# Kernel optimization log

Hardware: AMD Instinct MI355X
Metric: run time of the kernel (lower is better)

Reference implementation:

```python
import jax, jax.numpy as jnp
import numpy as np

T_STEPS = 200
B = 512
D = 32
LMBD = 1.0


def _socm_const_m_loss(ts, states, noises, controls, nabla_V, nabla_f,
                       nabla_b, nabla_g, sigma, log_pd, log_ps, log_tw):
    # ts: [T+1]; states/nabla_V: [T+1,B,D]; noises/controls/nabla_f: [T,B,D];
    # nabla_b: [T,B,D,D]; nabla_g: [B,D]; sigma: [D,D]; logs: [B]
    sigma_inv_T = jnp.linalg.inv(sigma).T

    # integrand terms on the first T timesteps ([:-1] slice in torch source)
    term1 = nabla_f  # nabla_f(ts[0], states)[:-1]
    sig_noises = jnp.einsum('ij,abj->abi', sigma_inv_T, noises)
    term2 = -np.sqrt(LMBD) * jnp.einsum('abij,abj->abi', nabla_b, sig_noises)
    sig_controls = jnp.einsum('ij,abj->abi', sigma_inv_T, controls)
    term3 = -jnp.einsum('abij,abj->abi', nabla_b, sig_controls)

    dts = ts[1:] - ts[:-1]                      # [T]
    dts_ = dts[:, None, None]
    zeros = jnp.zeros_like(term1[:1])           # [1,B,D]

    t1_dt = jnp.concatenate([zeros, term1 * dts_], axis=0)             # [T+1,B,D]
    t2_sdt = jnp.concatenate([zeros, term2 * jnp.sqrt(dts_)], axis=0)
    t3_dt = jnp.concatenate([zeros, term3 * dts_], axis=0)

    def rev_cum(x):
        # total_sum - cumsum == reverse cumulative sum starting at each step
        return jnp.sum(x, axis=0, keepdims=True) - jnp.cumsum(x, axis=0)

    least_squares_target = (rev_cum(t1_dt) + rev_cum(t2_sdt) + rev_cum(t3_dt)
                            + nabla_g[None, :, :])                     # [T+1,B,D]

    control_learned = -jnp.einsum('ij,tbj->tbi', sigma.T, nabla_V)
    control_target = -jnp.einsum('ij,tbj->tbi', sigma.T, least_squares_target)

    weight = jnp.exp(log_pd + log_ps + log_tw)  # [B]
    sq = (control_learned - control_target) ** 2 * weight[None, :, None]
    n_t, n_b = states.shape[0], states.shape[1]
    return jnp.sum(sq) / (n_t * n_b)


def setup_inputs() -> dict:
    key = jax.random.key(0)
    ks = jax.random.split(key, 11)
    ts = jnp.linspace(0.0, 1.0, T_STEPS + 1, dtype=jnp.float32)
    states = jax.random.normal(ks[0], (T_STEPS + 1, B, D), jnp.float32)
    noises = jax.random.normal(ks[1], (T_STEPS, B, D), jnp.float32)
    controls = jax.random.normal(ks[2], (T_STEPS, B, D), jnp.float32)
    nabla_V = jax.random.normal(ks[3], (T_STEPS + 1, B, D), jnp.float32)
    nabla_f = jax.random.normal(ks[4], (T_STEPS, B, D), jnp.float32)
    nabla_b = 0.1 * jax.random.normal(ks[5], (T_STEPS, B, D, D), jnp.float32)
    nabla_g = jax.random.normal(ks[6], (B, D), jnp.float32)
    sigma = jnp.eye(D, dtype=jnp.float32) + 0.05 * jax.random.normal(ks[7], (D, D), jnp.float32)
    log_pd = 0.01 * jax.random.normal(ks[8], (B,), jnp.float32)
    log_ps = 0.01 * jax.random.normal(ks[9], (B,), jnp.float32)
    log_tw = 0.01 * jax.random.normal(ks[10], (B,), jnp.float32)
    return {"ts": ts, "states": states, "noises": noises, "controls": controls,
            "nabla_V": nabla_V, "nabla_f": nabla_f, "nabla_b": nabla_b,
            "nabla_g": nabla_g, "sigma": sigma, "log_pd": log_pd,
            "log_ps": log_ps, "log_tw": log_tw}


def reference(ts, states, noises, controls, nabla_V, nabla_f, nabla_b,
              nabla_g, sigma, log_pd, log_ps, log_tw):
    return _socm_const_m_loss(ts, states, noises, controls, nabla_V, nabla_f,
                              nabla_b, nabla_g, sigma, log_pd, log_ps, log_tw)
```

## Files before the change

kernel.cpp:

```cpp
#include <hip/hip_runtime.h>
#include <math.h>

#define T_STEPS 200
#define BB 512
#define DD 32
#define LMBD 1.0f
#define NCH 8
#define CHT 25

#define WS_MINV 0
#define WS_A    1024
#define WS_W    2048
#define WS_PART 2560
#define WS_DT   3072
#define WS_SDT  3328
#define WS_CT   4096
#define WS_Y    135168
#define WS_M    266240

__global__ __launch_bounds__(512) void prep_kernel(
    const float* __restrict__ ts,
    const float* __restrict__ sigma,
    const float* __restrict__ lpd, const float* __restrict__ lps,
    const float* __restrict__ ltw,
    float* __restrict__ ws)
{
    __shared__ float sg[32][33];
    const int tid = threadIdx.x;

    ws[WS_W + tid] = expf(lpd[tid] + lps[tid] + ltw[tid]);

    if (tid < T_STEPS) {
        float a = ts[tid], b = ts[tid + 1];
        float dt = b - a;
        ws[WS_DT + tid]  = dt;
        ws[WS_SDT + tid] = sqrtf(LMBD * dt);
    }

    for (int idx = tid; idx < 1024; idx += 512)
        sg[idx >> 5][idx & 31] = sigma[idx];
    __syncthreads();

    for (int idx = tid; idx < 1024; idx += 512) {
        int i = idx >> 5, j = idx & 31;
        float s = 0.0f;
        #pragma unroll
        for (int k = 0; k < 32; ++k) s += sg[i][k] * sg[j][k];
        ws[WS_A + idx] = s;
    }

    if (tid < 64) {
        const int l = tid;
        float col[32];
        #pragma unroll
        for (int r = 0; r < 32; ++r) {
            float v = sg[r][l & 31];
            col[r] = (l < 32) ? v : ((r == (l - 32)) ? 1.0f : 0.0f);
        }
        #pragma unroll
        for (int k = 0; k < 32; ++k) {
            float pinv = 1.0f / __shfl(col[k], k);
            col[k] *= pinv;
            #pragma unroll
            for (int r = 0; r < 32; ++r) {
                if (r == k) continue;
                float f = __shfl(col[r], k);
                col[r] -= f * col[k];
            }
        }
        if (l >= 32) {
            #pragma unroll
            for (int r = 0; r < 32; ++r)
                ws[WS_MINV + (l - 32) * 32 + r] = col[r];
        }
    }
}

__global__ __launch_bounds__(64) void stream_kernel(
    const float* __restrict__ noises,
    const float* __restrict__ controls,
    const float* __restrict__ nabla_f,
    const float* __restrict__ nabla_V,
    const float* __restrict__ nabla_b,
    float* __restrict__ ws)
{
    const int h = blockIdx.x;
    const int b = blockIdx.y;
    const int l = threadIdx.x;
    const int j = l & 31;
    const int half = l >> 5;
    const int cg = l & 7;
    const int rg = l >> 3;

    const int t0 = h * CHT, t1 = t0 + CHT;

    float Mv[16];
    #pragma unroll
    for (int c = 0; c < 16; ++c)
        Mv[c] = ws[WS_MINV + j * 32 + 16 * half + c];

    const float* sm1p = (half == 0) ? noises  : controls;
    const float* sm2p = (half == 0) ? nabla_f : nabla_V;

    const float4* nb = (const float4*)nabla_b;

    size_t tf4 = (size_t)(t0 * BB + b) * 256;
    float4 n0 = nb[tf4 + l];
    float4 n1 = nb[tf4 + l + 64];
    float4 n2 = nb[tf4 + l + 128];
    float4 n3 = nb[tf4 + l + 192];
    float s1 = sm1p[(size_t)(t0 * BB + b) * DD + j];
    float s2 = sm2p[(size_t)(t0 * BB + b) * DD + j];

    float P = 0.0f, Yacc = 0.0f;
    float M00=0,M01=0,M02=0,M03=0, M10=0,M11=0,M12=0,M13=0;
    float M20=0,M21=0,M22=0,M23=0, M30=0,M31=0,M32=0,M33=0;

    for (int t = t0; t < t1; ++t) {
        const int tn = (t + 1 < t1) ? t + 1 : t;
        size_t tf4n = (size_t)(tn * BB + b) * 256;
        float4 m0 = nb[tf4n + l];
        float4 m1 = nb[tf4n + l + 64];
        float4 m2 = nb[tf4n + l + 128];
        float4 m3 = nb[tf4n + l + 192];
        float s1n = sm1p[(size_t)(tn * BB + b) * DD + j];
        float s2n = sm2p[(size_t)(tn * BB + b) * DD + j];

        const float dt  = ws[WS_DT + t];
        const float sdt = ws[WS_SDT + t];

        float o1 = __shfl_xor(s1, 32);
        float o2 = __shfl_xor(s2, 32);
        float nse = (half == 0) ? s1 : o1;
        float ctl = (half == 0) ? o1 : s1;
        float fv  = (half == 0) ? s2 : o2;
        float Vv  = (half == 0) ? o2 : s2;

        float w = -sdt * nse - dt * ctl;

        float part = 0.0f;
        #pragma unroll
        for (int c = 0; c < 16; ++c)
            part += Mv[c] * __shfl(w, 16 * half + c);
        float v = part + __shfl_xor(part, 32);

        float y = P + Vv;
        Yacc += y;

        float vg0 = __shfl(v, 4 * cg + 0);
        float vg1 = __shfl(v, 4 * cg + 1);
        float vg2 = __shfl(v, 4 * cg + 2);
        float vg3 = __shfl(v, 4 * cg + 3);
        float d0 = n0.x*vg0 + n0.y*vg1 + n0.z*vg2 + n0.w*vg3;
        float d1 = n1.x*vg0 + n1.y*vg1 + n1.z*vg2 + n1.w*vg3;
        float d2 = n2.x*vg0 + n2.y*vg1 + n2.z*vg2 + n2.w*vg3;
        float d3 = n3.x*vg0 + n3.y*vg1 + n3.z*vg2 + n3.w*vg3;
        d0 += __shfl_xor(d0,1); d0 += __shfl_xor(d0,2); d0 += __shfl_xor(d0,4);
        d1 += __shfl_xor(d1,1); d1 += __shfl_xor(d1,2); d1 += __shfl_xor(d1,4);
        d2 += __shfl_xor(d2,1); d2 += __shfl_xor(d2,2); d2 += __shfl_xor(d2,4);
        d3 += __shfl_xor(d3,1); d3 += __shfl_xor(d3,2); d3 += __shfl_xor(d3,4);
        float g0 = __shfl(d0, 8 * (l & 7));
        float g1 = __shfl(d1, 8 * (l & 7));
        float g2 = __shfl(d2, 8 * (l & 7));
        float g3 = __shfl(d3, 8 * (l & 7));
        const int slot = (l >> 3) & 3;
        float pA = (slot & 1) ? g1 : g0;
        float pB = (slot & 1) ? g3 : g2;
        float pc = (slot & 2) ? pB : pA;

        P += dt * fv + pc;

        float yr0 = __shfl(y, rg + 0);
        float yr1 = __shfl(y, rg + 8);
        float yr2 = __shfl(y, rg + 16);
        float yr3 = __shfl(y, rg + 24);
        float yc0 = __shfl(y, 4 * cg + 0);
        float yc1 = __shfl(y, 4 * cg + 1);
        float yc2 = __shfl(y, 4 * cg + 2);
        float yc3 = __shfl(y, 4 * cg + 3);
        M00 += yr0*yc0; M01 += yr0*yc1; M02 += yr0*yc2; M03 += yr0*yc3;
        M10 += yr1*yc0; M11 += yr1*yc1; M12 += yr1*yc2; M13 += yr1*yc3;
        M20 += yr2*yc0; M21 += yr2*yc1; M22 += yr2*yc2; M23 += yr2*yc3;
        M30 += yr3*yc0; M31 += yr3*yc1; M32 += yr3*yc2; M33 += yr3*yc3;

        n0 = m0; n1 = m1; n2 = m2; n3 = m3; s1 = s1n; s2 = s2n;
    }

    if (h == NCH - 1) {
        float Vt = nabla_V[((size_t)T_STEPS * BB + b) * DD + j];
        float y = P + Vt;
        Yacc += y;
        float yr0 = __shfl(y, rg + 0);
        float yr1 = __shfl(y, rg + 8);
        float yr2 = __shfl(y, rg + 16);
        float yr3 = __shfl(y, rg + 24);
        float yc0 = __shfl(y, 4 * cg + 0);
        float yc1 = __shfl(y, 4 * cg + 1);
        float yc2 = __shfl(y, 4 * cg + 2);
        float yc3 = __shfl(y, 4 * cg + 3);
        M00 += yr0*yc0; M01 += yr0*yc1; M02 += yr0*yc2; M03 += yr0*yc3;
        M10 += yr1*yc0; M11 += yr1*yc1; M12 += yr1*yc2; M13 += yr1*yc3;
        M20 += yr2*yc0; M21 += yr2*yc1; M22 += yr2*yc2; M23 += yr2*yc3;
        M30 += yr3*yc0; M31 += yr3*yc1; M32 += yr3*yc2; M33 += yr3*yc3;
    }

    float mpart = 0.0f;
    {
        const float* Ab = ws + WS_A;
        float4 A0 = *(const float4*)(Ab + (rg +  0) * 32 + 4 * cg);
        float4 A1 = *(const float4*)(Ab + (rg +  8) * 32 + 4 * cg);
        float4 A2 = *(const float4*)(Ab + (rg + 16) * 32 + 4 * cg);
        float4 A3 = *(const float4*)(Ab + (rg + 24) * 32 + 4 * cg);
        mpart = M00*A0.x + M01*A0.y + M02*A0.z + M03*A0.w
              + M10*A1.x + M11*A1.y + M12*A1.z + M13*A1.w
              + M20*A2.x + M21*A2.y + M22*A2.z + M23*A2.w
              + M30*A3.x + M31*A3.y + M32*A3.z + M33*A3.w;
    }
    mpart += __shfl_xor(mpart, 1);
    mpart += __shfl_xor(mpart, 2);
    mpart += __shfl_xor(mpart, 4);
    mpart += __shfl_xor(mpart, 8);
    mpart += __shfl_xor(mpart, 16);
    mpart += __shfl_xor(mpart, 32);

    if (half == 0) {
        ws[WS_CT + (b * NCH + h) * 32 + j] = P;
        ws[WS_Y  + (b * NCH + h) * 32 + j] = Yacc;
    }
    if (l == 0) ws[WS_M + b * NCH + h] = mpart;
}

__global__ __launch_bounds__(256) void combine_kernel(
    const float* __restrict__ nabla_g,
    float* __restrict__ ws)
{
    __shared__ float ct[NCH][32], Yl[NCH][32];
    __shared__ float Sv[32], Cp[32];
    __shared__ __align__(16) float sp[32];
    __shared__ float red[32];

    const int b   = blockIdx.x;
    const int tid = threadIdx.x;
    const int r   = tid >> 3;
    const int q   = tid & 7;

    {
        int hh = tid >> 5, i = tid & 31;
        ct[hh][i] = ws[WS_CT + (b * NCH + hh) * 32 + i];
        Yl[hh][i] = ws[WS_Y  + (b * NCH + hh) * 32 + i];
    }
    if (tid < 32) Cp[tid] = 0.0f;
    __syncthreads();
    if (tid < 32) {
        float s = nabla_g[b * 32 + tid];
        #pragma unroll
        for (int hh = 0; hh < NCH; ++hh) s += ct[hh][tid];
        Sv[tid] = s;
    }

    float acc = 0.0f;
    float4 A4 = *(const float4*)(ws + WS_A + r * 32 + 4 * q);
    for (int hh = 0; hh < NCH; ++hh) {
        __syncthreads();
        if (tid < 32) sp[tid] = Sv[tid] - Cp[tid];
        __syncthreads();
        float4 s4 = *(const float4*)&sp[4 * q];
        float as = A4.x * s4.x + A4.y * s4.y + A4.z * s4.z + A4.w * s4.w;
        as += __shfl_xor(as, 1);
        as += __shfl_xor(as, 2);
        as += __shfl_xor(as, 4);
        float nh = (hh == NCH - 1) ? (float)(CHT + 1) : (float)CHT;
        if (q == 0) acc += as * (nh * sp[r] - 2.0f * Yl[hh][r]);
        if (tid < 32) Cp[tid] += ct[hh][tid];
    }
    __syncthreads();
    if (q == 0) red[r] = acc;
    __syncthreads();
    if (tid == 0) {
        float s = 0.0f;
        #pragma unroll
        for (int i = 0; i < 32; ++i) s += red[i];
        #pragma unroll
        for (int hh = 0; hh < NCH; ++hh) s += ws[WS_M + b * NCH + hh];
        ws[WS_PART + b] = ws[WS_W + b] * s;
    }
}

__global__ __launch_bounds__(512) void reduce_kernel(
    const float* __restrict__ ws, float* __restrict__ out)
{
    __shared__ float r[512];
    const int tid = threadIdx.x;
    r[tid] = ws[WS_PART + tid];
    __syncthreads();
    for (int st = 256; st > 0; st >>= 1) {
        if (tid < st) r[tid] += r[tid + st];
        __syncthreads();
    }
    if (tid == 0) out[0] = r[0] * (1.0f / (201.0f * 512.0f));
}

extern "C" void kernel_launch(void* const* d_in, const int* in_sizes, int n_in,
                              void* d_out, int out_size, void* d_ws, size_t ws_size,
                              hipStream_t stream) {
    (void)in_sizes; (void)n_in; (void)out_size; (void)ws_size;
    const float* ts       = (const float*)d_in[0];
    const float* noises   = (const float*)d_in[2];
    const float* controls = (const float*)d_in[3];
    const float* nabla_V  = (const float*)d_in[4];
    const float* nabla_f  = (const float*)d_in[5];
    const float* nabla_b  = (const float*)d_in[6];
    const float* nabla_g  = (const float*)d_in[7];
    const float* sigma    = (const float*)d_in[8];
    const float* lpd      = (const float*)d_in[9];
    const float* lps      = (const float*)d_in[10];
    const float* ltw      = (const float*)d_in[11];
    float* ws  = (float*)d_ws;
    float* out = (float*)d_out;

    prep_kernel<<<1, 512, 0, stream>>>(ts, sigma, lpd, lps, ltw, ws);
    stream_kernel<<<dim3(NCH, BB), 64, 0, stream>>>(noises, controls, nabla_f,
                                                    nabla_V, nabla_b, ws);
    combine_kernel<<<BB, 256, 0, stream>>>(nabla_g, ws);
    reduce_kernel<<<1, 512, 0, stream>>>(ws, out);
}
```

Baseline: 115.2 us.

## Split sigma-inverse projection into separate kernel and double time chunks

Computes the projected noise/control vector v for every (t,b) in a new v_kernel and stores it in the workspace. The stream kernel then only reads v, nabla_f and nabla_V, with time cut into 16 chunks of 12-13 steps and four waves per block. This removes the per-step shuffle matvec from the serial loop and raises parallelism. The cost is an extra write and read of a T×B×D buffer and the loss of the manual next-step prefetch.

```diff
diff --git a/kernel.cpp b/kernel.cpp
--- a/kernel.cpp
+++ b/kernel.cpp
@@ -5,8 +5,7 @@
 #define BB 512
 #define DD 32
 #define LMBD 1.0f
-#define NCH 8
-#define CHT 25
+#define NCH 16
 
 #define WS_MINV 0
 #define WS_A    1024
@@ -14,9 +13,10 @@
 #define WS_PART 2560
 #define WS_DT   3072
 #define WS_SDT  3328
-#define WS_CT   4096
-#define WS_Y    135168
-#define WS_M    266240
+#define WS_V    4096
+#define WS_CT   3280896
+#define WS_Y    3543040
+#define WS_M    3805184
 
 __global__ __launch_bounds__(512) void prep_kernel(
     const float* __restrict__ ts,
@@ -76,85 +76,89 @@
     }
 }
 
-__global__ __launch_bounds__(64) void stream_kernel(
+__global__ __launch_bounds__(256) void v_kernel(
     const float* __restrict__ noises,
     const float* __restrict__ controls,
+    float* __restrict__ ws)
+{
+    __shared__ __align__(16) float wsm[8][36];
+    const int tid = threadIdx.x;
+    const int uu = tid >> 5, j = tid & 31;
+    const int unit = blockIdx.x * 8 + uu;
+    const int t = unit >> 9;
+
+    const float dt  = ws[WS_DT + t];
+    const float sdt = ws[WS_SDT + t];
+
+    const size_t g = (size_t)unit * DD + j;
+    float nv = noises[g], cv = controls[g];
+    wsm[uu][j] = -sdt * nv - dt * cv;
+
+    float4 mr[8];
+    {
+        const float4* mp = (const float4*)(ws + WS_MINV + j * 32);
+        #pragma unroll
+        for (int c = 0; c < 8; ++c) mr[c] = mp[c];
+    }
+    __syncthreads();
+
+    float v = 0.0f;
+    {
+        const float4* wr = (const float4*)wsm[uu];
+        #pragma unroll
+        for (int c = 0; c < 8; ++c) {
+            float4 a = wr[c];
+            v += mr[c].x * a.x + mr[c].y * a.y + mr[c].z * a.z + mr[c].w * a.w;
+        }
+    }
+    ws[WS_V + g] = v;
+}
+
+__global__ __launch_bounds__(256) void stream_kernel(
     const float* __restrict__ nabla_f,
     const float* __restrict__ nabla_V,
     const float* __restrict__ nabla_b,
     float* __restrict__ ws)
 {
-    const int h = blockIdx.x;
-    const int b = blockIdx.y;
-    const int l = threadIdx.x;
-    const int j = l & 31;
-    const int half = l >> 5;
-    const int cg = l & 7;
-    const int rg = l >> 3;
-
-    const int t0 = h * CHT, t1 = t0 + CHT;
-
-    float Mv[16];
-    #pragma unroll
-    for (int c = 0; c < 16; ++c)
-        Mv[c] = ws[WS_MINV + j * 32 + 16 * half + c];
-
-    const float* sm1p = (half == 0) ? noises  : controls;
-    const float* sm2p = (half == 0) ? nabla_f : nabla_V;
+    const int tid = threadIdx.x;
+    const int wv  = tid >> 6;
+    const int l   = tid & 63;
+    const int U   = blockIdx.x * 4 + wv;
+    const int b   = U >> 4;
+    const int h   = U & 15;
+    const int j   = l & 31;
+    const int cg  = l & 7;
+    const int rg  = l >> 3;
+
+    const int t0  = (h < 8) ? 13 * h : 104 + 12 * (h - 8);
+    const int len = (h < 8) ? 13 : 12;
+    const int t1  = t0 + len;
 
     const float4* nb = (const float4*)nabla_b;
-
-    size_t tf4 = (size_t)(t0 * BB + b) * 256;
-    float4 n0 = nb[tf4 + l];
-    float4 n1 = nb[tf4 + l + 64];
-    float4 n2 = nb[tf4 + l + 128];
-    float4 n3 = nb[tf4 + l + 192];
-    float s1 = sm1p[(size_t)(t0 * BB + b) * DD + j];
-    float s2 = sm2p[(size_t)(t0 * BB + b) * DD + j];
 
     float P = 0.0f, Yacc = 0.0f;
     float M00=0,M01=0,M02=0,M03=0, M10=0,M11=0,M12=0,M13=0;
     float M20=0,M21=0,M22=0,M23=0, M30=0,M31=0,M32=0,M33=0;
 
     for (int t = t0; t < t1; ++t) {
-        const int tn = (t + 1 < t1) ? t + 1 : t;
-        size_t tf4n = (size_t)(tn * BB + b) * 256;
-        float4 m0 = nb[tf4n + l];
-        float4 m1 = nb[tf4n + l + 64];
-        float4 m2 = nb[tf4n + l + 128];
-        float4 m3 = nb[tf4n + l + 192];
-        float s1n = sm1p[(size_t)(tn * BB + b) * DD + j];
-        float s2n = sm2p[(size_t)(tn * BB + b) * DD + j];
-
-        const float dt  = ws[WS_DT + t];
-        const float sdt = ws[WS_SDT + t];
-
-        float o1 = __shfl_xor(s1, 32);
-        float o2 = __shfl_xor(s2, 32);
-        float nse = (half == 0) ? s1 : o1;
-        float ctl = (half == 0) ? o1 : s1;
-        float fv  = (half == 0) ? s2 : o2;
-        float Vv  = (half == 0) ? o2 : s2;
-
-        float w = -sdt * nse - dt * ctl;
-
-        float part = 0.0f;
-        #pragma unroll
-        for (int c = 0; c < 16; ++c)
-            part += Mv[c] * __shfl(w, 16 * half + c);
-        float v = part + __shfl_xor(part, 32);
-
-        float y = P + Vv;
+        const int base = (t * BB + b) * DD;
+        const size_t f4 = (size_t)base * 8;
+        float4 n0 = nb[f4 + l];
+        float4 n1 = nb[f4 + l + 64];
+        float4 n2 = nb[f4 + l + 128];
+        float4 n3 = nb[f4 + l + 192];
+        float4 v4 = *(const float4*)(ws + WS_V + base + 4 * cg);
+        float fj  = nabla_f[base + j];
+        float Vj  = nabla_V[base + j];
+        float dt  = ws[WS_DT + t];
+
+        float y = P + Vj;
         Yacc += y;
 
-        float vg0 = __shfl(v, 4 * cg + 0);
-        float vg1 = __shfl(v, 4 * cg + 1);
-        float vg2 = __shfl(v, 4 * cg + 2);
-        float vg3 = __shfl(v, 4 * cg + 3);
-        float d0 = n0.x*vg0 + n0.y*vg1 + n0.z*vg2 + n0.w*vg3;
-        float d1 = n1.x*vg0 + n1.y*vg1 + n1.z*vg2 + n1.w*vg3;
-        float d2 = n2.x*vg0 + n2.y*vg1 + n2.z*vg2 + n2.w*vg3;
-        float d3 = n3.x*vg0 + n3.y*vg1 + n3.z*vg2 + n3.w*vg3;
+        float d0 = n0.x*v4.x + n0.y*v4.y + n0.z*v4.z + n0.w*v4.w;
+        float d1 = n1.x*v4.x + n1.y*v4.y + n1.z*v4.z + n1.w*v4.w;
+        float d2 = n2.x*v4.x + n2.y*v4.y + n2.z*v4.z + n2.w*v4.w;
+        float d3 = n3.x*v4.x + n3.y*v4.y + n3.z*v4.z + n3.w*v4.w;
         d0 += __shfl_xor(d0,1); d0 += __shfl_xor(d0,2); d0 += __shfl_xor(d0,4);
         d1 += __shfl_xor(d1,1); d1 += __shfl_xor(d1,2); d1 += __shfl_xor(d1,4);
         d2 += __shfl_xor(d2,1); d2 += __shfl_xor(d2,2); d2 += __shfl_xor(d2,4);
@@ -168,7 +172,7 @@
         float pB = (slot & 1) ? g3 : g2;
         float pc = (slot & 2) ? pB : pA;
 
-        P += dt * fv + pc;
+        P += dt * fj + pc;
 
         float yr0 = __shfl(y, rg + 0);
         float yr1 = __shfl(y, rg + 8);
@@ -182,8 +186,6 @@
         M10 += yr1*yc0; M11 += yr1*yc1; M12 += yr1*yc2; M13 += yr1*yc3;
         M20 += yr2*yc0; M21 += yr2*yc1; M22 += yr2*yc2; M23 += yr2*yc3;
         M30 += yr3*yc0; M31 += yr3*yc1; M32 += yr3*yc2; M33 += yr3*yc3;
-
-        n0 = m0; n1 = m1; n2 = m2; n3 = m3; s1 = s1n; s2 = s2n;
     }
 
     if (h == NCH - 1) {
@@ -204,7 +206,7 @@
         M30 += yr3*yc0; M31 += yr3*yc1; M32 += yr3*yc2; M33 += yr3*yc3;
     }
 
-    float mpart = 0.0f;
+    float mpart;
     {
         const float* Ab = ws + WS_A;
         float4 A0 = *(const float4*)(Ab + (rg +  0) * 32 + 4 * cg);
@@ -223,7 +225,7 @@
     mpart += __shfl_xor(mpart, 16);
     mpart += __shfl_xor(mpart, 32);
 
-    if (half == 0) {
+    if ((l >> 5) == 0) {
         ws[WS_CT + (b * NCH + h) * 32 + j] = P;
         ws[WS_Y  + (b * NCH + h) * 32 + j] = Yacc;
     }
@@ -244,8 +246,8 @@
     const int r   = tid >> 3;
     const int q   = tid & 7;
 
-    {
-        int hh = tid >> 5, i = tid & 31;
+    for (int idx = tid; idx < NCH * 32; idx += 256) {
+        int hh = idx >> 5, i = idx & 31;
         ct[hh][i] = ws[WS_CT + (b * NCH + hh) * 32 + i];
         Yl[hh][i] = ws[WS_Y  + (b * NCH + hh) * 32 + i];
     }
@@ -269,7 +271,7 @@
         as += __shfl_xor(as, 1);
         as += __shfl_xor(as, 2);
         as += __shfl_xor(as, 4);
-        float nh = (hh == NCH - 1) ? (float)(CHT + 1) : (float)CHT;
+        float nh = ((hh < 8) ? 13.0f : 12.0f) + ((hh == NCH - 1) ? 1.0f : 0.0f);
         if (q == 0) acc += as * (nh * sp[r] - 2.0f * Yl[hh][r]);
         if (tid < 32) Cp[tid] += ct[hh][tid];
     }
@@ -319,8 +321,9 @@
     float* out = (float*)d_out;
 
     prep_kernel<<<1, 512, 0, stream>>>(ts, sigma, lpd, lps, ltw, ws);
-    stream_kernel<<<dim3(NCH, BB), 64, 0, stream>>>(noises, controls, nabla_f,
-                                                    nabla_V, nabla_b, ws);
+    v_kernel<<<(T_STEPS * BB) / 8, 256, 0, stream>>>(noises, controls, ws);
+    stream_kernel<<<(BB * NCH) / 4, 256, 0, stream>>>(nabla_f, nabla_V,
+                                                      nabla_b, ws);
     combine_kernel<<<BB, 256, 0, stream>>>(nabla_g, ws);
     reduce_kernel<<<1, 512, 0, stream>>>(ws, out);
 }
```

Result: slower. 167.7 us (+45.6%).
